# Kernel optimization log

Hardware: AMD Instinct MI355X
Metric: run time of the kernel (lower is better)

The kernel has to match this reference:

```python
import jax, jax.numpy as jnp
import numpy as np

BS, TS, VOCAB, F = 8192, 100, 100000, 64

def _tri_idx(ts):
    # flat indices of strictly-upper-triangular entries of a ts x ts matrix
    i, j = np.triu_indices(ts, k=1)
    return jnp.asarray(i * ts + j)

def setup_inputs() -> dict:
    key = jax.random.key(0)
    ks = jax.random.split(key, 5)
    x = jax.random.randint(ks[0], (BS, TS), 0, VOCAB)
    emb = jax.random.normal(ks[1], (VOCAB, F), jnp.float32) * 0.02
    w_deep = jax.random.normal(ks[2], (F, F // 2), jnp.float32) * 0.05
    b_deep = jnp.zeros((F // 2,), jnp.float32)
    out_dim = TS * (TS - 1) // 2 + TS * (F // 2) + TS * F  # fm + deep + wide
    w_ffn = jax.random.normal(ks[3], (out_dim, 1), jnp.float32) * 0.01
    b_ffn = jnp.zeros((1,), jnp.float32)
    return {"x": x, "emb": emb, "w_deep": w_deep, "b_deep": b_deep,
            "w_ffn": w_ffn, "b_ffn": b_ffn}

def reference(x, emb, w_deep, b_deep, w_ffn, b_ffn):
    e = emb[x]                                  # [bs, ts, f]
    bs, ts, f = e.shape
    # pairwise dot products; keep only strictly-upper pairs (i<j)
    fm = jnp.einsum('btf,byf->bty', e, e)       # [bs, ts, ts]
    fm = fm.reshape(bs, ts * ts)[:, _tri_idx(ts)]   # [bs, ts*(ts-1)/2]
    deep = jax.nn.relu(e @ w_deep + b_deep).reshape(bs, -1)  # [bs, ts*f/2]
    wide = e.reshape(bs, ts * f)
    concat = jnp.concatenate([deep, fm, wide], axis=-1)
    return jax.nn.sigmoid(concat @ w_ffn + b_ffn)  # [bs, 1]
```

## Files before the change

### kernel.cpp

```cpp
#include <hip/hip_runtime.h>
#include <cmath>


#define TS 100
#define F  64
#define FD 32
#define RP 112
#define OFF_FM 3200
#define OFF_WIDE 8150
#define VOCAB 100000
#define W2_ELEMS (RP*RP)
#define W3_ELEMS (FD*RP)
#define WDT_ELEMS (FD*F)

typedef __attribute__((ext_vector_type(8))) short short8;
typedef __attribute__((ext_vector_type(4))) float f32x4;

constexpr int FM_TI[28] = {0,0,0,0,0,0,0, 1,1,1,1,1,1, 2,2,2,2,2, 3,3,3,3, 4,4,4, 5,5, 6};
constexpr int FM_TJ[28] = {0,1,2,3,4,5,6, 1,2,3,4,5,6, 2,3,4,5,6, 3,4,5,6, 4,5,6, 5,6, 6};

__device__ __forceinline__ ushort f2bf(float x) {
    uint u = __float_as_uint(x);
    u = (u + 0x7FFFu + ((u >> 16) & 1u)) >> 16;
    return (ushort)u;
}
__device__ __forceinline__ float bf2f(ushort h) {
    return __uint_as_float((uint)h << 16);
}

__global__ __launch_bounds__(256)
void emb_cvt(const float* __restrict__ src, ushort* __restrict__ dst, int n8) {
    int i = blockIdx.x * 256 + threadIdx.x;
    if (i >= n8) return;
    const float4* s = reinterpret_cast<const float4*>(src) + (size_t)i * 2;
    float4 a = s[0], b = s[1];
    ushort t[8] = { f2bf(a.x), f2bf(a.y), f2bf(a.z), f2bf(a.w),
                    f2bf(b.x), f2bf(b.y), f2bf(b.z), f2bf(b.w) };
    reinterpret_cast<uint4*>(dst)[i] = *reinterpret_cast<const uint4*>(t);
}

__global__ __launch_bounds__(256)
void prep(const float* __restrict__ w_ffn, const float* __restrict__ w_deep,
          float* __restrict__ W2, float* __restrict__ W3, ushort* __restrict__ wdt) {
    int j = blockIdx.x * 256 + threadIdx.x;
    if (j < W2_ELEMS) {
        int jc = j / RP, i = j % RP;
        float v = 0.f;
        if (i < jc && jc < TS)
            v = w_ffn[OFF_FM + i * (199 - i) / 2 + (jc - i - 1)];
        W2[j] = v;
    } else if (j < W2_ELEMS + W3_ELEMS) {
        int q = j - W2_ELEMS;
        int k = q / RP, t = q % RP;
        W3[q] = (t < TS) ? w_ffn[t * FD + k] : 0.f;
    } else if (j < W2_ELEMS + W3_ELEMS + WDT_ELEMS) {
        int q = j - W2_ELEMS - W3_ELEMS;
        int k = q >> 6, f = q & 63;
        wdt[q] = f2bf(w_deep[f * FD + k]);
    }
}

template<int W>
__device__ __forceinline__ float units(const char* esp, const char* wdp,
                                       int c0, int c1,
                                       const float* pW2, const float* pW3,
                                       const float* bdl) {
    float z = 0.f;
    #pragma unroll
    for (int u = W; u < 42; u += 4) {
        f32x4 acc = {0.f, 0.f, 0.f, 0.f};
        if (u < 28) {
            const int ti = FM_TI[u], tj = FM_TJ[u];
            short8 a0 = *reinterpret_cast<const short8*>(esp + ti * 2048 + c0);
            short8 a1 = *reinterpret_cast<const short8*>(esp + ti * 2048 + c1);
            short8 b0 = *reinterpret_cast<const short8*>(esp + tj * 2048 + c0);
            short8 b1 = *reinterpret_cast<const short8*>(esp + tj * 2048 + c1);
            acc = __builtin_amdgcn_mfma_f32_16x16x32_bf16(a0, b0, acc, 0, 0, 0);
            acc = __builtin_amdgcn_mfma_f32_16x16x32_bf16(a1, b1, acc, 0, 0, 0);
            float4 w = *reinterpret_cast<const float4*>(pW2 + tj * 1792 + ti * 16);
            z += acc[0] * w.x + acc[1] * w.y + acc[2] * w.z + acc[3] * w.w;
        } else {
            const int v = u - 28, tt = v >> 1, kt = v & 1;
            short8 a0 = *reinterpret_cast<const short8*>(esp + tt * 2048 + c0);
            short8 a1 = *reinterpret_cast<const short8*>(esp + tt * 2048 + c1);
            short8 b0 = *reinterpret_cast<const short8*>(wdp + kt * 2048 + c0);
            short8 b1 = *reinterpret_cast<const short8*>(wdp + kt * 2048 + c1);
            acc = __builtin_amdgcn_mfma_f32_16x16x32_bf16(a0, b0, acc, 0, 0, 0);
            acc = __builtin_amdgcn_mfma_f32_16x16x32_bf16(a1, b1, acc, 0, 0, 0);
            float bk = bdl[kt * 16];
            float4 w = *reinterpret_cast<const float4*>(pW3 + kt * 1792 + tt * 16);
            z += fmaxf(acc[0] + bk, 0.f) * w.x + fmaxf(acc[1] + bk, 0.f) * w.y
               + fmaxf(acc[2] + bk, 0.f) * w.z + fmaxf(acc[3] + bk, 0.f) * w.w;
        }
    }
    return z;
}

template<bool EMBBF>
__global__ __launch_bounds__(256)
void deepfm_main(const int* __restrict__ x,
                 const float* __restrict__ embf,
                 const ushort* __restrict__ embh,
                 const float* __restrict__ W2,
                 const float* __restrict__ W3,
                 const ushort* __restrict__ wdt,
                 const float* __restrict__ b_deep,
                 const float* __restrict__ w_ffn,
                 const float* __restrict__ b_ffn,
                 float* __restrict__ out)
{
    __shared__ ushort Es[RP * F];
    __shared__ ushort wdT[FD * F];
    __shared__ float  bdeep_lds[FD];
    __shared__ int    xs[TS];
    __shared__ float  red[4];

    const int tid  = threadIdx.x;
    const int b    = blockIdx.x;
    const int lane = tid & 63;
    const int wave = tid >> 6;
    const int lr   = lane & 15;
    const int lg   = lane >> 4;

    if (tid < TS) xs[tid] = x[(size_t)b * TS + tid];
    if (tid < FD) bdeep_lds[tid] = b_deep[tid];
    {
        int k = tid >> 3, k8 = tid & 7;
        int col = (k8 * 16) ^ ((k & 7) << 4);
        *reinterpret_cast<uint4*>(reinterpret_cast<char*>(wdT) + k * 128 + col)
            = *reinterpret_cast<const uint4*>(wdt + k * F + k8 * 8);
    }
    __syncthreads();

    for (int j = tid; j < RP * 8; j += 256) {
        int r = j >> 3, k8 = j & 7;
        int col = (k8 * 16) ^ ((r & 7) << 4);
        char* dst = reinterpret_cast<char*>(Es) + r * 128 + col;
        if (r < TS) {
            if (EMBBF) {
                *reinterpret_cast<uint4*>(dst) =
                    *reinterpret_cast<const uint4*>(embh + (size_t)xs[r] * F + k8 * 8);
            } else {
                const float* s = embf + (size_t)xs[r] * F + k8 * 8;
                float4 a = reinterpret_cast<const float4*>(s)[0];
                float4 c = reinterpret_cast<const float4*>(s)[1];
                ushort t[8] = { f2bf(a.x), f2bf(a.y), f2bf(a.z), f2bf(a.w),
                                f2bf(c.x), f2bf(c.y), f2bf(c.z), f2bf(c.w) };
                *reinterpret_cast<uint4*>(dst) = *reinterpret_cast<const uint4*>(t);
            }
        } else {
            *reinterpret_cast<uint4*>(dst) = make_uint4(0, 0, 0, 0);
        }
    }
    __syncthreads();

    const int sw = (lr & 7) << 4;
    const int c0 = (lg * 16) ^ sw;
    const int c1 = (64 + lg * 16) ^ sw;
    const char* esp = reinterpret_cast<const char*>(Es) + lr * 128;
    const char* wdp = reinterpret_cast<const char*>(wdT) + lr * 128;
    const float* pW2 = W2 + lr * RP + lg * 4;
    const float* pW3 = W3 + lr * RP + lg * 4;
    const float* bdl = bdeep_lds + lr;

    float z;
    switch (wave) {
        case 0:  z = units<0>(esp, wdp, c0, c1, pW2, pW3, bdl); break;
        case 1:  z = units<1>(esp, wdp, c0, c1, pW2, pW3, bdl); break;
        case 2:  z = units<2>(esp, wdp, c0, c1, pW2, pW3, bdl); break;
        default: z = units<3>(esp, wdp, c0, c1, pW2, pW3, bdl); break;
    }

    for (int j = tid; j < TS * 8; j += 256) {
        int t = j >> 3, k8 = j & 7;
        int off = (k8 * 16) ^ ((t & 7) << 4);
        short8 v = *reinterpret_cast<const short8*>(
            reinterpret_cast<const char*>(Es) + t * 128 + off);
        const float2* w = reinterpret_cast<const float2*>(w_ffn + OFF_WIDE + t * F + k8 * 8);
        float2 wa = w[0], wb = w[1], wc = w[2], wd = w[3];
        z += bf2f((ushort)v[0]) * wa.x + bf2f((ushort)v[1]) * wa.y
           + bf2f((ushort)v[2]) * wb.x + bf2f((ushort)v[3]) * wb.y
           + bf2f((ushort)v[4]) * wc.x + bf2f((ushort)v[5]) * wc.y
           + bf2f((ushort)v[6]) * wd.x + bf2f((ushort)v[7]) * wd.y;
    }

    #pragma unroll
    for (int off = 32; off > 0; off >>= 1) z += __shfl_down(z, off, 64);
    if ((tid & 63) == 0) red[wave] = z;
    __syncthreads();
    if (tid == 0) {
        float t = red[0] + red[1] + red[2] + red[3] + b_ffn[0];
        out[b] = 1.f / (1.f + expf(-t));
    }
}

extern "C" void kernel_launch(void* const* d_in, const int* in_sizes, int n_in,
                              void* d_out, int out_size, void* d_ws, size_t ws_size,
                              hipStream_t stream) {
    const int*   x      = (const int*)  d_in[0];
    const float* emb    = (const float*)d_in[1];
    const float* w_deep = (const float*)d_in[2];
    const float* b_deep = (const float*)d_in[3];
    const float* w_ffn  = (const float*)d_in[4];
    const float* b_ffn  = (const float*)d_in[5];
    float* out = (float*)d_out;
    const int bs = in_sizes[0] / TS;
    const size_t embh_bytes = (size_t)VOCAB * F * 2;
    const size_t w2_bytes = W2_ELEMS * 4;
    const size_t w3_bytes = W3_ELEMS * 4;
    const size_t wdt_bytes = WDT_ELEMS * 2;
    const size_t wtot = w2_bytes + w3_bytes + wdt_bytes;
    const int prep_jobs = W2_ELEMS + W3_ELEMS + WDT_ELEMS;

    if (ws_size >= embh_bytes + wtot) {
        ushort* embhp = (ushort*)d_ws;
        float*  W2p   = (float*)((char*)d_ws + embh_bytes);
        float*  W3p   = (float*)((char*)d_ws + embh_bytes + w2_bytes);
        ushort* wdtp  = (ushort*)((char*)d_ws + embh_bytes + w2_bytes + w3_bytes);
        const int n8 = VOCAB * F / 8;
        hipLaunchKernelGGL(emb_cvt, dim3((n8 + 255) / 256), dim3(256), 0, stream,
                           emb, embhp, n8);
        hipLaunchKernelGGL(prep, dim3((prep_jobs + 255) / 256), dim3(256), 0, stream,
                           w_ffn, w_deep, W2p, W3p, wdtp);
        hipLaunchKernelGGL((deepfm_main<true>), dim3(bs), dim3(256), 0, stream,
                           x, emb, embhp, W2p, W3p, wdtp, b_deep, w_ffn, b_ffn, out);
    } else {
        float*  W2p  = (float*)d_ws;
        float*  W3p  = (float*)((char*)d_ws + w2_bytes);
        ushort* wdtp = (ushort*)((char*)d_ws + w2_bytes + w3_bytes);
        hipLaunchKernelGGL(prep, dim3((prep_jobs + 255) / 256), dim3(256), 0, stream,
                           w_ffn, w_deep, W2p, W3p, wdtp);
        hipLaunchKernelGGL((deepfm_main<false>), dim3(bs), dim3(256), 0, stream,
                           x, emb, (const ushort*)nullptr, W2p, W3p, wdtp,
                           b_deep, w_ffn, b_ffn, out);
    }
}
```

Measured before the change: 158.9 us.

## Process eight samples per block with double-buffered embedding gather

Each block now handles G=8 batch rows and prefetches the next row's embedding gather into registers while computing the current one, then writes it to a second LDS buffer. The wide-term dot product is computed from the registers during the gather, so the LDS re-read is gone. FM and deep work is reorganised into strips per wave so A/B fragments are reused across MFMAs. Fewer blocks and setup costs are amortised, but grid parallelism drops to bs/8 blocks and correctness assumes bs is divisible by 8.

Measured after the change: 179.5 us. +12.9%, slower.

```diff
diff --git a/kernel.cpp b/kernel.cpp
--- a/kernel.cpp
+++ b/kernel.cpp
@@ -6,18 +6,17 @@
 #define F  64
 #define FD 32
 #define RP 112
+#define G  8
 #define OFF_FM 3200
 #define OFF_WIDE 8150
 #define VOCAB 100000
 #define W2_ELEMS (RP*RP)
 #define W3_ELEMS (FD*RP)
 #define WDT_ELEMS (FD*F)
+#define ESTRIDE (RP*F)
 
 typedef __attribute__((ext_vector_type(8))) short short8;
 typedef __attribute__((ext_vector_type(4))) float f32x4;
-
-constexpr int FM_TI[28] = {0,0,0,0,0,0,0, 1,1,1,1,1,1, 2,2,2,2,2, 3,3,3,3, 4,4,4, 5,5, 6};
-constexpr int FM_TJ[28] = {0,1,2,3,4,5,6, 1,2,3,4,5,6, 2,3,4,5,6, 3,4,5,6, 4,5,6, 5,6, 6};
 
 __device__ __forceinline__ ushort f2bf(float x) {
     uint u = __float_as_uint(x);
@@ -60,44 +59,78 @@
     }
 }
 
-template<int W>
-__device__ __forceinline__ float units(const char* esp, const char* wdp,
-                                       int c0, int c1,
-                                       const float* pW2, const float* pW3,
-                                       const float* bdl) {
+template<int TI>
+__device__ __forceinline__ float fm_strip(const char* esp, int c0, int c1,
+                                          const float* pW2) {
+    short8 A0 = *reinterpret_cast<const short8*>(esp + TI * 2048 + c0);
+    short8 A1 = *reinterpret_cast<const short8*>(esp + TI * 2048 + c1);
     float z = 0.f;
     #pragma unroll
-    for (int u = W; u < 42; u += 4) {
+    for (int tj = TI; tj < 7; ++tj) {
+        short8 B0, B1;
+        if (tj == TI) { B0 = A0; B1 = A1; }
+        else {
+            B0 = *reinterpret_cast<const short8*>(esp + tj * 2048 + c0);
+            B1 = *reinterpret_cast<const short8*>(esp + tj * 2048 + c1);
+        }
         f32x4 acc = {0.f, 0.f, 0.f, 0.f};
-        if (u < 28) {
-            const int ti = FM_TI[u], tj = FM_TJ[u];
-            short8 a0 = *reinterpret_cast<const short8*>(esp + ti * 2048 + c0);
-            short8 a1 = *reinterpret_cast<const short8*>(esp + ti * 2048 + c1);
-            short8 b0 = *reinterpret_cast<const short8*>(esp + tj * 2048 + c0);
-            short8 b1 = *reinterpret_cast<const short8*>(esp + tj * 2048 + c1);
-            acc = __builtin_amdgcn_mfma_f32_16x16x32_bf16(a0, b0, acc, 0, 0, 0);
-            acc = __builtin_amdgcn_mfma_f32_16x16x32_bf16(a1, b1, acc, 0, 0, 0);
-            float4 w = *reinterpret_cast<const float4*>(pW2 + tj * 1792 + ti * 16);
-            z += acc[0] * w.x + acc[1] * w.y + acc[2] * w.z + acc[3] * w.w;
-        } else {
-            const int v = u - 28, tt = v >> 1, kt = v & 1;
-            short8 a0 = *reinterpret_cast<const short8*>(esp + tt * 2048 + c0);
-            short8 a1 = *reinterpret_cast<const short8*>(esp + tt * 2048 + c1);
-            short8 b0 = *reinterpret_cast<const short8*>(wdp + kt * 2048 + c0);
-            short8 b1 = *reinterpret_cast<const short8*>(wdp + kt * 2048 + c1);
-            acc = __builtin_amdgcn_mfma_f32_16x16x32_bf16(a0, b0, acc, 0, 0, 0);
-            acc = __builtin_amdgcn_mfma_f32_16x16x32_bf16(a1, b1, acc, 0, 0, 0);
-            float bk = bdl[kt * 16];
-            float4 w = *reinterpret_cast<const float4*>(pW3 + kt * 1792 + tt * 16);
-            z += fmaxf(acc[0] + bk, 0.f) * w.x + fmaxf(acc[1] + bk, 0.f) * w.y
-               + fmaxf(acc[2] + bk, 0.f) * w.z + fmaxf(acc[3] + bk, 0.f) * w.w;
-        }
+        acc = __builtin_amdgcn_mfma_f32_16x16x32_bf16(A0, B0, acc, 0, 0, 0);
+        acc = __builtin_amdgcn_mfma_f32_16x16x32_bf16(A1, B1, acc, 0, 0, 0);
+        float4 w = *reinterpret_cast<const float4*>(pW2 + tj * 1792 + TI * 16);
+        z += acc[0] * w.x + acc[1] * w.y + acc[2] * w.z + acc[3] * w.w;
     }
     return z;
 }
 
+template<int KT>
+__device__ __forceinline__ float deep_strip(const char* esp, const char* wdp,
+                                            int c0, int c1, const float* pW3,
+                                            float bk) {
+    short8 B0 = *reinterpret_cast<const short8*>(wdp + KT * 2048 + c0);
+    short8 B1 = *reinterpret_cast<const short8*>(wdp + KT * 2048 + c1);
+    float z = 0.f;
+    #pragma unroll
+    for (int tt = 0; tt < 7; ++tt) {
+        short8 A0 = *reinterpret_cast<const short8*>(esp + tt * 2048 + c0);
+        short8 A1 = *reinterpret_cast<const short8*>(esp + tt * 2048 + c1);
+        f32x4 acc = {0.f, 0.f, 0.f, 0.f};
+        acc = __builtin_amdgcn_mfma_f32_16x16x32_bf16(A0, B0, acc, 0, 0, 0);
+        acc = __builtin_amdgcn_mfma_f32_16x16x32_bf16(A1, B1, acc, 0, 0, 0);
+        float4 w = *reinterpret_cast<const float4*>(pW3 + KT * 1792 + tt * 16);
+        z += fmaxf(acc[0] + bk, 0.f) * w.x + fmaxf(acc[1] + bk, 0.f) * w.y
+           + fmaxf(acc[2] + bk, 0.f) * w.z + fmaxf(acc[3] + bk, 0.f) * w.w;
+    }
+    return z;
+}
+
 template<bool EMBBF>
-__global__ __launch_bounds__(256)
+__device__ __forceinline__ uint4 load8(const float* __restrict__ embf,
+                                       const ushort* __restrict__ embh,
+                                       int xr, int k8) {
+    if (EMBBF) {
+        return *reinterpret_cast<const uint4*>(embh + (size_t)xr * F + k8 * 8);
+    } else {
+        const float* s = embf + (size_t)xr * F + k8 * 8;
+        float4 a = reinterpret_cast<const float4*>(s)[0];
+        float4 c = reinterpret_cast<const float4*>(s)[1];
+        ushort t[8] = { f2bf(a.x), f2bf(a.y), f2bf(a.z), f2bf(a.w),
+                        f2bf(c.x), f2bf(c.y), f2bf(c.z), f2bf(c.w) };
+        return *reinterpret_cast<const uint4*>(t);
+    }
+}
+
+__device__ __forceinline__ float dotj(uint4 v, const float* __restrict__ w) {
+    short8 sv = *reinterpret_cast<const short8*>(&v);
+    const float2* w2 = reinterpret_cast<const float2*>(w);
+    float2 wa = w2[0], wb = w2[1], wc = w2[2], wd = w2[3];
+    return bf2f((ushort)sv[0]) * wa.x + bf2f((ushort)sv[1]) * wa.y
+         + bf2f((ushort)sv[2]) * wb.x + bf2f((ushort)sv[3]) * wb.y
+         + bf2f((ushort)sv[4]) * wc.x + bf2f((ushort)sv[5]) * wc.y
+         + bf2f((ushort)sv[6]) * wd.x + bf2f((ushort)sv[7]) * wd.y;
+}
+
+template<bool EMBBF>
+__global__ __launch_bounds__(256, 4)
 void deepfm_main(const int* __restrict__ x,
                  const float* __restrict__ embf,
                  const ushort* __restrict__ embh,
@@ -109,21 +142,19 @@
                  const float* __restrict__ b_ffn,
                  float* __restrict__ out)
 {
-    __shared__ ushort Es[RP * F];
+    __shared__ ushort Es[2][ESTRIDE];
     __shared__ ushort wdT[FD * F];
-    __shared__ float  bdeep_lds[FD];
-    __shared__ int    xs[TS];
-    __shared__ float  red[4];
+    __shared__ int    xsa[G * TS];
+    __shared__ float  red[G][4];
 
     const int tid  = threadIdx.x;
-    const int b    = blockIdx.x;
     const int lane = tid & 63;
     const int wave = tid >> 6;
     const int lr   = lane & 15;
     const int lg   = lane >> 4;
-
-    if (tid < TS) xs[tid] = x[(size_t)b * TS + tid];
-    if (tid < FD) bdeep_lds[tid] = b_deep[tid];
+    const int b0   = blockIdx.x * G;
+
+    for (int j = tid; j < G * TS; j += 256) xsa[j] = x[(size_t)b0 * TS + j];
     {
         int k = tid >> 3, k8 = tid & 7;
         int col = (k8 * 16) ^ ((k & 7) << 4);
@@ -132,65 +163,86 @@
     }
     __syncthreads();
 
-    for (int j = tid; j < RP * 8; j += 256) {
-        int r = j >> 3, k8 = j & 7;
-        int col = (k8 * 16) ^ ((r & 7) << 4);
-        char* dst = reinterpret_cast<char*>(Es) + r * 128 + col;
-        if (r < TS) {
-            if (EMBBF) {
-                *reinterpret_cast<uint4*>(dst) =
-                    *reinterpret_cast<const uint4*>(embh + (size_t)xs[r] * F + k8 * 8);
-            } else {
-                const float* s = embf + (size_t)xs[r] * F + k8 * 8;
-                float4 a = reinterpret_cast<const float4*>(s)[0];
-                float4 c = reinterpret_cast<const float4*>(s)[1];
-                ushort t[8] = { f2bf(a.x), f2bf(a.y), f2bf(a.z), f2bf(a.w),
-                                f2bf(c.x), f2bf(c.y), f2bf(c.z), f2bf(c.w) };
-                *reinterpret_cast<uint4*>(dst) = *reinterpret_cast<const uint4*>(t);
-            }
-        } else {
-            *reinterpret_cast<uint4*>(dst) = make_uint4(0, 0, 0, 0);
-        }
-    }
-    __syncthreads();
-
-    const int sw = (lr & 7) << 4;
-    const int c0 = (lg * 16) ^ sw;
-    const int c1 = (64 + lg * 16) ^ sw;
-    const char* esp = reinterpret_cast<const char*>(Es) + lr * 128;
+    const int k8  = tid & 7;
+    const int r0  = tid >> 3;
+    const int sw  = (r0 & 7) << 4;
+    const int col = (k8 * 16) ^ sw;
+    const bool has3  = tid < 128;
+    const bool real3 = tid < 32;
+    const float* ww0 = w_ffn + OFF_WIDE + (r0)      * F + k8 * 8;
+    const float* ww1 = w_ffn + OFF_WIDE + (r0 + 32) * F + k8 * 8;
+    const float* ww2 = w_ffn + OFF_WIDE + (r0 + 64) * F + k8 * 8;
+    const float* ww3 = real3 ? (w_ffn + OFF_WIDE + (r0 + 96) * F + k8 * 8) : nullptr;
+
+    const int c0 = (lg * 16) ^ ((lr & 7) << 4);
+    const int c1 = (64 + lg * 16) ^ ((lr & 7) << 4);
     const char* wdp = reinterpret_cast<const char*>(wdT) + lr * 128;
     const float* pW2 = W2 + lr * RP + lg * 4;
     const float* pW3 = W3 + lr * RP + lg * 4;
-    const float* bdl = bdeep_lds + lr;
-
-    float z;
-    switch (wave) {
-        case 0:  z = units<0>(esp, wdp, c0, c1, pW2, pW3, bdl); break;
-        case 1:  z = units<1>(esp, wdp, c0, c1, pW2, pW3, bdl); break;
-        case 2:  z = units<2>(esp, wdp, c0, c1, pW2, pW3, bdl); break;
-        default: z = units<3>(esp, wdp, c0, c1, pW2, pW3, bdl); break;
-    }
-
-    for (int j = tid; j < TS * 8; j += 256) {
-        int t = j >> 3, k8 = j & 7;
-        int off = (k8 * 16) ^ ((t & 7) << 4);
-        short8 v = *reinterpret_cast<const short8*>(
-            reinterpret_cast<const char*>(Es) + t * 128 + off);
-        const float2* w = reinterpret_cast<const float2*>(w_ffn + OFF_WIDE + t * F + k8 * 8);
-        float2 wa = w[0], wb = w[1], wc = w[2], wd = w[3];
-        z += bf2f((ushort)v[0]) * wa.x + bf2f((ushort)v[1]) * wa.y
-           + bf2f((ushort)v[2]) * wb.x + bf2f((ushort)v[3]) * wb.y
-           + bf2f((ushort)v[4]) * wc.x + bf2f((ushort)v[5]) * wc.y
-           + bf2f((ushort)v[6]) * wd.x + bf2f((ushort)v[7]) * wd.y;
-    }
-
-    #pragma unroll
-    for (int off = 32; off > 0; off >>= 1) z += __shfl_down(z, off, 64);
-    if ((tid & 63) == 0) red[wave] = z;
+    const float bk0 = b_deep[lr];
+    const float bk1 = b_deep[16 + lr];
+
+    float zw_pend;
+    {
+        uint4 v0 = load8<EMBBF>(embf, embh, xsa[r0], k8);
+        uint4 v1 = load8<EMBBF>(embf, embh, xsa[r0 + 32], k8);
+        uint4 v2 = load8<EMBBF>(embf, embh, xsa[r0 + 64], k8);
+        uint4 v3 = make_uint4(0, 0, 0, 0);
+        if (real3) v3 = load8<EMBBF>(embf, embh, xsa[r0 + 96], k8);
+        zw_pend = dotj(v0, ww0) + dotj(v1, ww1) + dotj(v2, ww2);
+        if (real3) zw_pend += dotj(v3, ww3);
+        char* base = reinterpret_cast<char*>(Es[0]);
+        *reinterpret_cast<uint4*>(base + (r0)      * 128 + col) = v0;
+        *reinterpret_cast<uint4*>(base + (r0 + 32) * 128 + col) = v1;
+        *reinterpret_cast<uint4*>(base + (r0 + 64) * 128 + col) = v2;
+        if (has3) *reinterpret_cast<uint4*>(base + (r0 + 96) * 128 + col) = v3;
+    }
     __syncthreads();
-    if (tid == 0) {
-        float t = red[0] + red[1] + red[2] + red[3] + b_ffn[0];
-        out[b] = 1.f / (1.f + expf(-t));
+
+    for (int g = 0; g < G; ++g) {
+        const int cur = g & 1;
+        uint4 v0, v1, v2, v3 = make_uint4(0, 0, 0, 0);
+        if (g < G - 1) {
+            const int* xg = xsa + (g + 1) * TS;
+            v0 = load8<EMBBF>(embf, embh, xg[r0], k8);
+            v1 = load8<EMBBF>(embf, embh, xg[r0 + 32], k8);
+            v2 = load8<EMBBF>(embf, embh, xg[r0 + 64], k8);
+            if (real3) v3 = load8<EMBBF>(embf, embh, xg[r0 + 96], k8);
+        }
+
+        const char* esp = reinterpret_cast<const char*>(Es[cur]) + lr * 128;
+        float z = zw_pend;
+        switch (wave) {
+            case 0: z += fm_strip<0>(esp, c0, c1, pW2)
+                       + fm_strip<4>(esp, c0, c1, pW2); break;
+            case 1: z += fm_strip<1>(esp, c0, c1, pW2)
+                       + fm_strip<5>(esp, c0, c1, pW2)
+                       + fm_strip<6>(esp, c0, c1, pW2); break;
+            case 2: z += fm_strip<2>(esp, c0, c1, pW2)
+                       + deep_strip<0>(esp, wdp, c0, c1, pW3, bk0); break;
+            default: z += fm_strip<3>(esp, c0, c1, pW2)
+                       + deep_strip<1>(esp, wdp, c0, c1, pW3, bk1); break;
+        }
+
+        if (g < G - 1) {
+            zw_pend = dotj(v0, ww0) + dotj(v1, ww1) + dotj(v2, ww2);
+            if (real3) zw_pend += dotj(v3, ww3);
+            char* base = reinterpret_cast<char*>(Es[cur ^ 1]);
+            *reinterpret_cast<uint4*>(base + (r0)      * 128 + col) = v0;
+            *reinterpret_cast<uint4*>(base + (r0 + 32) * 128 + col) = v1;
+            *reinterpret_cast<uint4*>(base + (r0 + 64) * 128 + col) = v2;
+            if (has3) *reinterpret_cast<uint4*>(base + (r0 + 96) * 128 + col) = v3;
+        }
+
+        #pragma unroll
+        for (int off = 32; off > 0; off >>= 1) z += __shfl_down(z, off, 64);
+        if (lane == 0) red[g][wave] = z;
+        __syncthreads();
+    }
+
+    if (tid < G) {
+        float s = red[tid][0] + red[tid][1] + red[tid][2] + red[tid][3] + b_ffn[0];
+        out[b0 + tid] = 1.f / (1.f + expf(-s));
     }
 }
 
@@ -205,6 +257,7 @@
     const float* b_ffn  = (const float*)d_in[5];
     float* out = (float*)d_out;
     const int bs = in_sizes[0] / TS;
+    const int nblk = bs / G;
     const size_t embh_bytes = (size_t)VOCAB * F * 2;
     const size_t w2_bytes = W2_ELEMS * 4;
     const size_t w3_bytes = W3_ELEMS * 4;
@@ -222,7 +275,7 @@
                            emb, embhp, n8);
         hipLaunchKernelGGL(prep, dim3((prep_jobs + 255) / 256), dim3(256), 0, stream,
                            w_ffn, w_deep, W2p, W3p, wdtp);
-        hipLaunchKernelGGL((deepfm_main<true>), dim3(bs), dim3(256), 0, stream,
+        hipLaunchKernelGGL((deepfm_main<true>), dim3(nblk), dim3(256), 0, stream,
                            x, emb, embhp, W2p, W3p, wdtp, b_deep, w_ffn, b_ffn, out);
     } else {
         float*  W2p  = (float*)d_ws;
@@ -230,7 +283,7 @@
         ushort* wdtp = (ushort*)((char*)d_ws + w2_bytes + w3_bytes);
         hipLaunchKernelGGL(prep, dim3((prep_jobs + 255) / 256), dim3(256), 0, stream,
                            w_ffn, w_deep, W2p, W3p, wdtp);
-        hipLaunchKernelGGL((deepfm_main<false>), dim3(bs), dim3(256), 0, stream,
+        hipLaunchKernelGGL((deepfm_main<false>), dim3(nblk), dim3(256), 0, stream,
                            x, emb, (const ushort*)nullptr, W2p, W3p, wdtp,
                            b_deep, w_ffn, b_ffn, out);
     }
```
